# Kernel optimization log

Hardware: AMD Instinct MI355X
Metric: run time of the kernel (lower is better)

## Reference

```python
import jax, jax.numpy as jnp
import numpy as np
from jax import lax

BLANK = 0
B, T, U, V = 8, 256, 64, 512  # U1 = U + 1


def setup_inputs() -> dict:
    key = jax.random.key(0)
    k1, k2, k3 = jax.random.split(key, 3)
    enc_state = jax.random.normal(k1, (B, T, V), dtype=jnp.float32)
    dec_state = jax.random.normal(k2, (B, U + 1, V), dtype=jnp.float32)
    # targets are non-blank labels in [1, V)
    targets = jax.random.randint(k3, (B, U), 1, V, dtype=jnp.int32)
    input_lengths = jnp.full((B,), T, dtype=jnp.int32)
    target_lengths = jnp.full((B,), U, dtype=jnp.int32)
    return {"enc_state": enc_state, "dec_state": dec_state, "targets": targets,
            "input_lengths": input_lengths, "target_lengths": target_lengths}


def rnnt_loss(logits, targets, input_lengths, target_lengths, blank=BLANK):
    # logits: [B, T, U1, V]; targets: [B, U]
    b, t_len, u1, v = logits.shape
    u_len = u1 - 1
    lp = jax.nn.log_softmax(logits, axis=-1)
    blank_lp = lp[..., blank]                                   # [B, T, U1]
    idx = jnp.broadcast_to(targets[:, None, :, None], (b, t_len, u_len, 1))
    emit_lp = jnp.take_along_axis(lp[:, :, :u_len, :], idx, axis=3)[..., 0]  # [B, T, U]

    # alpha[0, u] = sum_{k<u} emit_lp[0, k]
    alpha0 = jnp.concatenate(
        [jnp.zeros((b, 1), lp.dtype), jnp.cumsum(emit_lp[:, 0, :], axis=1)], axis=1)  # [B, U1]

    def t_step(alpha_prev, xs):
        blank_prev, emit_t = xs  # [B, U1], [B, U]
        init = alpha_prev + blank_prev  # contribution from (t-1, u) blank transition

        def u_step(carry, x):
            init_u, emit_u = x  # each [B]
            a = jnp.logaddexp(init_u, carry + emit_u)  # a[u] = lse(init[u], a[u-1]+emit[u-1])
            return a, a

        _, rest = lax.scan(u_step, init[:, 0], (init[:, 1:].T, emit_t.T))  # rest: [U, B]
        alpha_t = jnp.concatenate([init[:, :1], rest.T], axis=1)  # [B, U1]
        return alpha_t, alpha_t

    xs = (blank_lp[:, :t_len - 1].transpose(1, 0, 2), emit_lp[:, 1:].transpose(1, 0, 2))
    _, alphas_rest = lax.scan(t_step, alpha0, xs)
    alphas = jnp.concatenate([alpha0[None], alphas_rest], axis=0)  # [T, B, U1]

    bi = jnp.arange(b)
    tl = target_lengths.astype(jnp.int32)
    il = input_lengths.astype(jnp.int32)
    a_final = alphas[il - 1, bi, tl]
    final_blank = blank_lp[bi, il - 1, tl]
    nll = -(a_final + final_blank)
    return jnp.mean(nll)  # reduction='mean'


def reference(enc_state, dec_state, targets, input_lengths, target_lengths):
    # JointNet: broadcast-add enc [B,T,1,V] + dec [B,1,U1,V] -> logits [B,T,U1,V]
    logits = enc_state[:, :, None, :] + dec_state[:, None, :, :]
    return rnnt_loss(logits, targets, input_lengths, target_lengths, blank=BLANK)
```

## Files before the change

kernel.cpp:

```cpp
#include <hip/hip_runtime.h>

#define B_ 8
#define T_ 256
#define U_ 64
#define U1_ 65
#define V_ 512
#define NDIAGP_ 336
#define NT_ 2
#define CH_ 64

#define LOG2E_ 1.4426950408889634f
#define LN2_   0.6931471805599453f

#if __has_builtin(__builtin_amdgcn_exp2f)
#define EXP2(x) __builtin_amdgcn_exp2f(x)
#else
#define EXP2(x) exp2f(x)
#endif

__global__ __launch_bounds__(256) void k_exp(const float* __restrict__ x,
                                             float* __restrict__ y, int n4,
                                             float* __restrict__ out)
{
    int i = blockIdx.x * blockDim.x + threadIdx.x;
    if (i == 0) out[0] = 0.0f;
    if (i < n4) {
        float4 v = ((const float4*)x)[i];
        float4 r;
        r.x = __expf(v.x); r.y = __expf(v.y);
        r.z = __expf(v.z); r.w = __expf(v.w);
        ((float4*)y)[i] = r;
    }
}

template <int CTRL, int RM>
__device__ __forceinline__ float dppadd(float x) {
    return x + __int_as_float(__builtin_amdgcn_update_dpp(
        0, __float_as_int(x), CTRL, RM, 0xf, true));
}
__device__ __forceinline__ float wave_sum64(float x) {
    x = dppadd<0x111, 0xf>(x);
    x = dppadd<0x112, 0xf>(x);
    x = dppadd<0x114, 0xf>(x);
    x = dppadd<0x118, 0xf>(x);
    x = dppadd<0x142, 0xa>(x);
    x = dppadd<0x143, 0xc>(x);
    return x;
}

__global__ __launch_bounds__(256) void k_logprobs(
    const float* __restrict__ enc, const float* __restrict__ dec,
    const float* __restrict__ edec, const int* __restrict__ targets,
    float* __restrict__ BLD, float* __restrict__ EMD)
{
    const int blk  = blockIdx.x;
    const int b    = blk % B_;
    const int tg   = blk / B_;
    const int t0   = tg * NT_;
    const int wave = threadIdx.x >> 6;
    const int lane = threadIdx.x & 63;

    float4 xe0[NT_], xe1[NT_];
    float  er0[NT_];
    #pragma unroll
    for (int j = 0; j < NT_; ++j) {
        const float* erow = enc + (size_t)(b * T_ + t0 + j) * V_;
        float4 e0 = *(const float4*)(erow + lane * 4);
        float4 e1 = *(const float4*)(erow + 256 + lane * 4);
        xe0[j].x = __expf(e0.x); xe0[j].y = __expf(e0.y);
        xe0[j].z = __expf(e0.z); xe0[j].w = __expf(e0.w);
        xe1[j].x = __expf(e1.x); xe1[j].y = __expf(e1.y);
        xe1[j].z = __expf(e1.z); xe1[j].w = __expf(e1.w);
        er0[j] = erow[0];
    }

    for (int u = wave; u <= U_; u += 4) {
        const float* xdrow = edec + (size_t)(b * U1_ + u) * V_;
        float4 d0 = *(const float4*)(xdrow + lane * 4);
        float4 d1 = *(const float4*)(xdrow + 256 + lane * 4);

        float s[NT_];
        #pragma unroll
        for (int j = 0; j < NT_; ++j) {
            float sA = xe0[j].x * d0.x;
            float sB = xe1[j].x * d1.x;
            sA = fmaf(xe0[j].y, d0.y, sA);  sB = fmaf(xe1[j].y, d1.y, sB);
            sA = fmaf(xe0[j].z, d0.z, sA);  sB = fmaf(xe1[j].z, d1.z, sB);
            sA = fmaf(xe0[j].w, d0.w, sA);  sB = fmaf(xe1[j].w, d1.w, sB);
            s[j] = sA + sB;
        }

        #pragma unroll
        for (int j = 0; j < NT_; ++j)
            s[j] = wave_sum64(s[j]);

        if (lane == 63) {
            const float* dr = dec + (size_t)(b * U1_ + u) * V_;
            const float d_blank = dr[0];
            int   tgt = 0;
            float d_tgt = 0.0f;
            if (u < U_) { tgt = targets[b * U_ + u]; d_tgt = dr[tgt]; }
            #pragma unroll
            for (int j = 0; j < NT_; ++j) {
                const int t  = t0 + j;
                const int dg = t + u;
                const float lse2 = log2f(s[j]);
                BLD[((size_t)b * NDIAGP_ + dg) * U1_ + u] =
                    (er0[j] + d_blank) * LOG2E_ - lse2;
                if (u < U_) {
                    const float* er = enc + (size_t)(b * T_ + t) * V_;
                    EMD[((size_t)b * NDIAGP_ + dg) * U_ + u] =
                        (er[tgt] + d_tgt) * LOG2E_ - lse2;
                }
            }
        }
    }
}

__device__ __forceinline__ float wshr1(float x) {
    return __int_as_float(__builtin_amdgcn_update_dpp(
        0, __float_as_int(x), 0x138, 0xf, 0xf, true));
}
template <int CTRL>
__device__ __forceinline__ float dppmax(float x) {
    return fmaxf(x, __int_as_float(__builtin_amdgcn_update_dpp(
        0, __float_as_int(x), CTRL, 0xf, 0xf, false)));
}
__device__ __forceinline__ float wave_max64(float x) {
    x = dppmax<0x111>(x);
    x = dppmax<0x112>(x);
    x = dppmax<0x114>(x);
    x = dppmax<0x118>(x);
    x = dppmax<0x142>(x);
    x = dppmax<0x143>(x);
    return __int_as_float(__builtin_amdgcn_readlane(__float_as_int(x), 63));
}

#define GLDS(c_) do {                                                           \
    if (wave > 0) {                                                             \
        const float* gbl = BLb + (size_t)(c_) * CH_ * U1_;                      \
        const float* gem = EMb + (size_t)(c_) * CH_ * U_;                       \
        float* lbl_ = sRBL[(c_) & 1];                                           \
        float* lem_ = sREM[(c_) & 1];                                           \
        for (int i = wave - 1; i < 17; i += 3)                                  \
            __builtin_amdgcn_global_load_lds(                                   \
                (const __attribute__((address_space(1))) void*)(gbl + i * 256 + lane * 4), \
                (__attribute__((address_space(3))) void*)(lbl_ + i * 256), 16, 0, 0);      \
        for (int i = wave - 1; i < 16; i += 3)                                  \
            __builtin_amdgcn_global_load_lds(                                   \
                (const __attribute__((address_space(1))) void*)(gem + i * 256 + lane * 4), \
                (__attribute__((address_space(3))) void*)(lem_ + i * 256), 16, 0, 0);      \
    }                                                                           \
} while (0)

#define CONV(c_) do {                                                           \
    if (wave > 0) {                                                             \
        const float* rbl = sRBL[(c_) & 1];                                      \
        const float* rem = sREM[(c_) & 1];                                      \
        float2* pv_ = sPV[(c_) & 1];                                            \
        float*  pc_ = sPC[(c_) & 1];                                            \
        _Pragma("unroll 4")                                                     \
        for (int i = wave - 1; i < CH_; i += 3) {                               \
            const float bl = rbl[i * U1_ + lane + 1];                           \
            const float em = rem[i * U_ + lane];                                \
            const float pc = ((c_) == 4) ? rbl[i * U1_ + i + 1]                 \
                                         : rbl[i * U1_];                        \
            float vb = fminf(bl - pc, 126.0f);                                  \
            float ve = fminf(em - pc, 126.0f);                                  \
            if ((c_) == 0 && lane == i) vb = -200.0f;                           \
            if ((c_) == 4 && lane <= i) { vb = -200.0f; ve = -200.0f; }         \
            pv_[i * 64 + lane] = make_float2(EXP2(vb), EXP2(ve));               \
            if (lane == 0) pc_[i] = pc;                                         \
        }                                                                       \
    }                                                                           \
} while (0)

#define LOADG(PV, PC, g_) do {                                                  \
    _Pragma("unroll")                                                           \
    for (int j = 0; j < 8; ++j) {                                               \
        PV[j] = pvb[(8 * (g_) + j) * 64 + lane];                                \
        PC[j] = pcb[8 * (g_) + j];                                              \
    }                                                                           \
} while (0)

#define COMPG(PV, PC, g_) do {                                                  \
    _Pragma("unroll")                                                           \
    for (int j = 0; j < 8; ++j) {                                               \
        const int d = d0 + 8 * (g_) + j + 1;                                    \
        float sr = wshr1(r);                                                    \
        sr = lane0 ? r0 : sr;                                                   \
        r = fmaf(sr, PV[j].y, r * PV[j].x);                                     \
        const bool cap = (d == cap_d);                                          \
        savedV = cap ? (tlpos ? r : r0) : savedV;                               \
        savedC = cap ? (tlpos ? Rc + PC[j] : Rc) : savedC;                      \
        Rc += PC[j];                                                            \
    }                                                                           \
    {                                                                           \
        float m = wave_max64(r);                                                \
        int mb = __float_as_int(m);                                             \
        int e = (mb >> 23) - 127;                                               \
        e = (mb >= 0x00800000) ? e : 0;                                         \
        float sc = __int_as_float((127 - e) << 23);                             \
        r *= sc;  r0 *= sc;  Rc += (float)e;                                    \
    }                                                                           \
} while (0)

#define CHUNK_BODY(c_) do {                                                     \
    const float2* pvb = sPV[(c_) & 1];                                          \
    const float*  pcb = sPC[(c_) & 1];                                          \
    const int d0 = CH_ * (c_);                                                  \
    float2 pvA[8], pvB[8];                                                      \
    float  pcA[8], pcB[8];                                                      \
    LOADG(pvA, pcA, 0);                                                         \
    for (int g = 0; g < 8; g += 2) {                                            \
        LOADG(pvB, pcB, g + 1);                                                 \
        COMPG(pvA, pcA, g);                                                     \
        if (g + 2 < 8) LOADG(pvA, pcA, g + 2);                                  \
        COMPG(pvB, pcB, g + 1);                                                 \
    }                                                                           \
} while (0)

__global__ __launch_bounds__(256) void k_alpha(
    const float* __restrict__ BLD, const float* __restrict__ EMD,
    const int* __restrict__ il_, const int* __restrict__ tl_,
    float* __restrict__ sink)
{
    __shared__ __align__(16) float  sRBL[2][17 * 256];
    __shared__ __align__(16) float  sREM[2][16 * 256];
    __shared__ __align__(16) float2 sPV[2][CH_ * 64];
    __shared__ float sPC[2][CH_];

    const int b    = blockIdx.x;
    const int wave = threadIdx.x >> 6;
    const int lane = threadIdx.x & 63;
    const int il   = il_[b];
    const int tl   = tl_[b];
    const int dstar = il - 1 + tl;
    const float* BLb = BLD + (size_t)b * NDIAGP_ * U1_;
    const float* EMb = EMD + (size_t)b * NDIAGP_ * U_;
    const float fblank = BLb[(size_t)dstar * U1_ + tl];

    const bool lane0 = (lane == 0);
    const bool tlpos = (tl > 0);
    const int  cap_d = tlpos ? dstar : il;

    float r  = 0.0f;
    float r0 = 1.0f;
    float Rc = 0.0f;
    float savedV = 1.0f, savedC = 0.0f;

    GLDS(0);
    __syncthreads();
    GLDS(1);
    CONV(0);
    __syncthreads();

    for (int c = 0; c < 5; ++c) {
        if (c + 2 <= 4) GLDS(c + 2);
        if (c + 1 <= 4) CONV(c + 1);
        if (wave == 0) { CHUNK_BODY(c); }
        __syncthreads();
    }

    if (wave == 0) {
        const int sl = tlpos ? (tl - 1) : 0;
        float sv = __int_as_float(
            __builtin_amdgcn_readlane(__float_as_int(savedV), sl));
        float sc = __int_as_float(
            __builtin_amdgcn_readlane(__float_as_int(savedC), 0));
        if (lane == 0)
            atomicAdd(sink, -(sc + log2f(sv) + fblank) * (LN2_ / B_));
    }
}

extern "C" void kernel_launch(void* const* d_in, const int* in_sizes, int n_in,
                              void* d_out, int out_size, void* d_ws, size_t ws_size,
                              hipStream_t stream)
{
    const float* enc     = (const float*)d_in[0];
    const float* dec     = (const float*)d_in[1];
    const int*   targets = (const int*)d_in[2];
    const int*   il      = (const int*)d_in[3];
    const int*   tl      = (const int*)d_in[4];
    float*       out     = (float*)d_out;

    float* edec = (float*)d_ws;
    float* BLD  = edec + (size_t)B_ * U1_ * V_;
    float* EMD  = BLD  + (size_t)B_ * NDIAGP_ * U1_;

    const int n4 = B_ * U1_ * V_ / 4;
    k_exp<<<(n4 + 255) / 256, 256, 0, stream>>>(dec, edec, n4, out);
    k_logprobs<<<B_ * T_ / NT_, 256, 0, stream>>>(enc, dec, edec, targets, BLD, EMD);
    k_alpha<<<B_, 256, 0, stream>>>(BLD, EMD, il, tl, out);
}
```

Measured before the change: 44.55 us.

## Use 8 waves in alpha kernel and pack transition factors as float4

Grows the alpha recursion block from 4 to 8 waves, so seven helper waves instead of three prefetch and convert each diagonal chunk into exp-space transition factors. The per-diagonal factor pairs are packed two per float4 and the cumulative-scale values are read as float4, which halves the number of LDS loads the serial recursion wave issues per diagonal. The aim is to shorten the producer stage and the LDS latency on the critical serial path. The cost is more threads per block and possible contention with the serial wave.

```diff
diff --git a/kernel.cpp b/kernel.cpp
--- a/kernel.cpp
+++ b/kernel.cpp
@@ -8,6 +8,7 @@
 #define NDIAGP_ 336
 #define NT_ 2
 #define CH_ 64
+#define AW_ 8
 
 #define LOG2E_ 1.4426950408889634f
 #define LN2_   0.6931471805599453f
@@ -142,11 +143,11 @@
         const float* gem = EMb + (size_t)(c_) * CH_ * U_;                       \
         float* lbl_ = sRBL[(c_) & 1];                                           \
         float* lem_ = sREM[(c_) & 1];                                           \
-        for (int i = wave - 1; i < 17; i += 3)                                  \
+        for (int i = wave - 1; i < 17; i += 7)                                  \
             __builtin_amdgcn_global_load_lds(                                   \
                 (const __attribute__((address_space(1))) void*)(gbl + i * 256 + lane * 4), \
                 (__attribute__((address_space(3))) void*)(lbl_ + i * 256), 16, 0, 0);      \
-        for (int i = wave - 1; i < 16; i += 3)                                  \
+        for (int i = wave - 1; i < 16; i += 7)                                  \
             __builtin_amdgcn_global_load_lds(                                   \
                 (const __attribute__((address_space(1))) void*)(gem + i * 256 + lane * 4), \
                 (__attribute__((address_space(3))) void*)(lem_ + i * 256), 16, 0, 0);      \
@@ -157,10 +158,10 @@
     if (wave > 0) {                                                             \
         const float* rbl = sRBL[(c_) & 1];                                      \
         const float* rem = sREM[(c_) & 1];                                      \
-        float2* pv_ = sPV[(c_) & 1];                                            \
+        float4* pv_ = sPV[(c_) & 1];                                            \
         float*  pc_ = sPC[(c_) & 1];                                            \
-        _Pragma("unroll 4")                                                     \
-        for (int i = wave - 1; i < CH_; i += 3) {                               \
+        _Pragma("unroll 3")                                                     \
+        for (int i = wave - 1; i < CH_; i += 7) {                               \
             const float bl = rbl[i * U1_ + lane + 1];                           \
             const float em = rem[i * U_ + lane];                                \
             const float pc = ((c_) == 4) ? rbl[i * U1_ + i + 1]                 \
@@ -169,31 +170,40 @@
             float ve = fminf(em - pc, 126.0f);                                  \
             if ((c_) == 0 && lane == i) vb = -200.0f;                           \
             if ((c_) == 4 && lane <= i) { vb = -200.0f; ve = -200.0f; }         \
-            pv_[i * 64 + lane] = make_float2(EXP2(vb), EXP2(ve));               \
+            ((float2*)&pv_[(i >> 1) * 64 + lane])[i & 1] =                      \
+                make_float2(EXP2(vb), EXP2(ve));                                \
             if (lane == 0) pc_[i] = pc;                                         \
         }                                                                       \
     }                                                                           \
 } while (0)
 
-#define LOADG(PV, PC, g_) do {                                                  \
+#define LOADG(PV, PCQ, g_) do {                                                 \
     _Pragma("unroll")                                                           \
-    for (int j = 0; j < 8; ++j) {                                               \
-        PV[j] = pvb[(8 * (g_) + j) * 64 + lane];                                \
-        PC[j] = pcb[8 * (g_) + j];                                              \
-    }                                                                           \
-} while (0)
-
-#define COMPG(PV, PC, g_) do {                                                  \
+    for (int k = 0; k < 4; ++k)                                                 \
+        PV[k] = pvb[(4 * (g_) + k) * 64 + lane];                                \
+    PCQ[0] = pcb4[2 * (g_)];                                                    \
+    PCQ[1] = pcb4[2 * (g_) + 1];                                                \
+} while (0)
+
+#define PCSEL(PCQ, j_) ((j_) < 4 ? ((j_) == 0 ? PCQ[0].x : (j_) == 1 ? PCQ[0].y \
+                                  : (j_) == 2 ? PCQ[0].z : PCQ[0].w)            \
+                                 : ((j_) == 4 ? PCQ[1].x : (j_) == 5 ? PCQ[1].y \
+                                  : (j_) == 6 ? PCQ[1].z : PCQ[1].w))
+
+#define COMPG(PV, PCQ, g_) do {                                                 \
     _Pragma("unroll")                                                           \
     for (int j = 0; j < 8; ++j) {                                               \
         const int d = d0 + 8 * (g_) + j + 1;                                    \
+        const float pbv = (j & 1) ? PV[j >> 1].z : PV[j >> 1].x;                \
+        const float pev = (j & 1) ? PV[j >> 1].w : PV[j >> 1].y;                \
+        const float pcj = PCSEL(PCQ, j);                                        \
         float sr = wshr1(r);                                                    \
         sr = lane0 ? r0 : sr;                                                   \
-        r = fmaf(sr, PV[j].y, r * PV[j].x);                                     \
+        r = fmaf(sr, pev, r * pbv);                                             \
         const bool cap = (d == cap_d);                                          \
         savedV = cap ? (tlpos ? r : r0) : savedV;                               \
-        savedC = cap ? (tlpos ? Rc + PC[j] : Rc) : savedC;                      \
-        Rc += PC[j];                                                            \
+        savedC = cap ? (tlpos ? Rc + pcj : Rc) : savedC;                        \
+        Rc += pcj;                                                              \
     }                                                                           \
     {                                                                           \
         float m = wave_max64(r);                                                \
@@ -206,11 +216,11 @@
 } while (0)
 
 #define CHUNK_BODY(c_) do {                                                     \
-    const float2* pvb = sPV[(c_) & 1];                                          \
-    const float*  pcb = sPC[(c_) & 1];                                          \
+    const float4* pvb  = sPV[(c_) & 1];                                         \
+    const float4* pcb4 = (const float4*)sPC[(c_) & 1];                          \
     const int d0 = CH_ * (c_);                                                  \
-    float2 pvA[8], pvB[8];                                                      \
-    float  pcA[8], pcB[8];                                                      \
+    float4 pvA[4], pvB[4];                                                      \
+    float4 pcA[2], pcB[2];                                                      \
     LOADG(pvA, pcA, 0);                                                         \
     for (int g = 0; g < 8; g += 2) {                                            \
         LOADG(pvB, pcB, g + 1);                                                 \
@@ -220,15 +230,15 @@
     }                                                                           \
 } while (0)
 
-__global__ __launch_bounds__(256) void k_alpha(
+__global__ __launch_bounds__(512) void k_alpha(
     const float* __restrict__ BLD, const float* __restrict__ EMD,
     const int* __restrict__ il_, const int* __restrict__ tl_,
     float* __restrict__ sink)
 {
     __shared__ __align__(16) float  sRBL[2][17 * 256];
     __shared__ __align__(16) float  sREM[2][16 * 256];
-    __shared__ __align__(16) float2 sPV[2][CH_ * 64];
-    __shared__ float sPC[2][CH_];
+    __shared__ __align__(16) float4 sPV[2][32 * 64];
+    __shared__ __align__(16) float  sPC[2][CH_];
 
     const int b    = blockIdx.x;
     const int wave = threadIdx.x >> 6;
@@ -291,5 +301,5 @@
     const int n4 = B_ * U1_ * V_ / 4;
     k_exp<<<(n4 + 255) / 256, 256, 0, stream>>>(dec, edec, n4, out);
     k_logprobs<<<B_ * T_ / NT_, 256, 0, stream>>>(enc, dec, edec, targets, BLD, EMD);
-    k_alpha<<<B_, 256, 0, stream>>>(BLD, EMD, il, tl, out);
-}
+    k_alpha<<<B_, 512, 0, stream>>>(BLD, EMD, il, tl, out);
+}
```

After: 40.50 us. -9.1%, faster.
